# Optimization experiments

Measured on AMD Instinct MI355X. Metric: run time of the kernel, lower is better.

The kernel has to match this reference:

```python
import jax, jax.numpy as jnp
import numpy as np

B, N, OBS = 512, 64, 256
H1, H2 = 4, 4
D = 128            # embed/key dim (d_k_1 = d_k_2 = 128)
O1 = D // H1       # 32, per-head value dim stage 1
O2 = D // H2       # 32, per-head value dim stage 2
IN2 = O1 * H1      # 128, input dim to stage 2
FOUT = 16          # final_output_dim


def setup_inputs() -> dict:
    key = jax.random.key(0)
    ks = jax.random.split(key, 22)
    g = lambda k, shp: (jax.random.normal(k, shp, dtype=jnp.float32) * 0.05)
    inp = {
        "states": jax.random.normal(ks[0], (B, N, OBS), dtype=jnp.float32),
        # stage 1 per-head params, stacked over heads
        "E1_w": g(ks[1], (H1, D, OBS)), "E1_b": g(ks[2], (H1, D)),
        "K1_w": g(ks[3], (H1, D, D)),   "K1_b": g(ks[4], (H1, D)),
        "Q1_w": g(ks[5], (H1, D, D)),   "Q1_b": g(ks[6], (H1, D)),
        "V1_w": g(ks[7], (H1, O1, D)),  "V1_b": g(ks[8], (H1, O1)),
        # stage 2 per-head params
        "E2_w": g(ks[9], (H2, D, IN2)), "E2_b": g(ks[10], (H2, D)),
        "K2_w": g(ks[11], (H2, D, D)),  "K2_b": g(ks[12], (H2, D)),
        "Q2_w": g(ks[13], (H2, D, D)),  "Q2_b": g(ks[14], (H2, D)),
        "V2_w": g(ks[15], (H2, O2, D)), "V2_b": g(ks[16], (H2, O2)),
        # final MLP policy head
        "F1_w": g(ks[17], (64, O2 * H2)), "F1_b": g(ks[18], (64,)),
        "F2_w": g(ks[19], (FOUT, 64)),    "F2_b": g(ks[20], (FOUT,)),
    }
    return inp


def _attn_block(x, Ew, Eb, Kw, Kb, Qw, Qb, Vw, Vb, d_k):
    # x: [B,N,I]; all head loops batched via leading head axis h
    se = jax.nn.leaky_relu(jnp.einsum('bni,hdi->hbnd', x, Ew) + Eb[:, None, None, :])  # [h,B,N,D]
    k = jnp.einsum('hbnd,hed->hbne', se, Kw) + Kb[:, None, None, :]
    q = jnp.einsum('hbnd,hed->hbne', se, Qw) + Qb[:, None, None, :]
    w = jax.nn.softmax(jnp.einsum('hbne,hbme->hbnm', q, k) / jnp.sqrt(jnp.float32(d_k)), axis=-1)  # [h,B,N,N]
    v = jax.nn.leaky_relu(jnp.einsum('hbnd,hod->hbno', se, Vw) + Vb[:, None, None, :])  # [h,B,N,O]
    att = jnp.einsum('hbnm,hbmo->hbno', w, v)
    h, b, n, o = att.shape
    return jnp.transpose(att, (1, 2, 0, 3)).reshape(b, n, h * o), w


def reference(states, E1_w, E1_b, K1_w, K1_b, Q1_w, Q1_b, V1_w, V1_b,
              E2_w, E2_b, K2_w, K2_b, Q2_w, Q2_b, V2_w, V2_b,
              F1_w, F1_b, F2_w, F2_b):
    x1, w1 = _attn_block(states, E1_w, E1_b, K1_w, K1_b, Q1_w, Q1_b, V1_w, V1_b, D)
    x2, w2 = _attn_block(x1, E2_w, E2_b, K2_w, K2_b, Q2_w, Q2_b, V2_w, V2_b, D)
    h = jax.nn.leaky_relu(jnp.einsum('bnf,of->bno', x2, F1_w) + F1_b)
    policy = jax.nn.softmax(jnp.einsum('bno,po->bnp', h, F2_w) + F2_b, axis=-1)
    return policy, w1, w2
```

## Files before the change

kernel.cpp:

```cpp
#include <hip/hip_runtime.h>

typedef __attribute__((ext_vector_type(8))) short short8;
typedef __attribute__((ext_vector_type(4))) short short4v;
typedef __attribute__((ext_vector_type(4))) float f32x4;
typedef __attribute__((ext_vector_type(2))) unsigned uint2v;

#define MFMA(a, b, c) __builtin_amdgcn_mfma_f32_16x16x32_bf16((a), (b), (c), 0, 0, 0)

__device__ __forceinline__ short f2bf(float f) {
    union { float f; unsigned u; } v; v.f = f;
    unsigned r = v.u + 0x7fffu + ((v.u >> 16) & 1u);
    return (short)(r >> 16);
}
__device__ __forceinline__ float bf2f(short s) {
    union { unsigned u; float f; } v; v.u = ((unsigned)(unsigned short)s) << 16; return v.f;
}
__device__ __forceinline__ unsigned pkbf(float lo, float hi) {
    return (unsigned)(unsigned short)f2bf(lo) | ((unsigned)(unsigned short)f2bf(hi) << 16);
}
__device__ __forceinline__ float lrelu(float v) { return (v >= 0.f) ? v : 0.01f * v; }

struct ConvArgs { const float* src[6]; int end[6]; };

__global__ __launch_bounds__(256) void convert_weights_kernel(ConvArgs a, short* __restrict__ dstw) {
    int i4 = blockIdx.x * 256 + threadIdx.x;
    int seg = 0;
#pragma unroll
    for (int s = 0; s < 5; s++) seg += (i4 >= a.end[s]) ? 1 : 0;
    int base = (seg == 0) ? 0 : a.end[seg - 1];
    float4 v = ((const float4*)a.src[seg])[i4 - base];
    uint2v o = { pkbf(v.x, v.y), pkbf(v.z, v.w) };
    *(uint2v*)(dstw + (size_t)i4 * 4) = o;
}

__global__ __launch_bounds__(256) void precompute_gt_kernel(
    const float* __restrict__ Q1w, const float* __restrict__ K1w, const float* __restrict__ Q1b,
    const float* __restrict__ Q2w, const float* __restrict__ K2w, const float* __restrict__ Q2b,
    short* __restrict__ gt, float* __restrict__ wvec) {
    const int s  = blockIdx.x >> 5;
    const int h  = (blockIdx.x >> 3) & 3;
    const int fg = blockIdx.x & 7;
    const float* Qw = (s ? Q2w : Q1w) + (size_t)h * 16384;
    const float* Kw = (s ? K2w : K1w) + (size_t)h * 16384;
    const float* qb = (s ? Q2b : Q1b) + h * 128;
    const int f  = fg * 16 + (threadIdx.x >> 4);
    const int e0 = (threadIdx.x & 15) * 8;
    float acc[8] = {0.f, 0.f, 0.f, 0.f, 0.f, 0.f, 0.f, 0.f};
    float accw = 0.f;
#pragma unroll 4
    for (int c = 0; c < 128; c++) {
        float kv = Kw[c * 128 + f];
        accw = fmaf(qb[c], kv, accw);
        float4 a0 = *(const float4*)(Qw + c * 128 + e0);
        float4 a1 = *(const float4*)(Qw + c * 128 + e0 + 4);
        acc[0] = fmaf(kv, a0.x, acc[0]); acc[1] = fmaf(kv, a0.y, acc[1]);
        acc[2] = fmaf(kv, a0.z, acc[2]); acc[3] = fmaf(kv, a0.w, acc[3]);
        acc[4] = fmaf(kv, a1.x, acc[4]); acc[5] = fmaf(kv, a1.y, acc[5]);
        acc[6] = fmaf(kv, a1.z, acc[6]); acc[7] = fmaf(kv, a1.w, acc[7]);
    }
    const float scale = 0.08838834764831845f;
    short8 o = { f2bf(acc[0] * scale), f2bf(acc[1] * scale), f2bf(acc[2] * scale), f2bf(acc[3] * scale),
                 f2bf(acc[4] * scale), f2bf(acc[5] * scale), f2bf(acc[6] * scale), f2bf(acc[7] * scale) };
    *(short8*)(gt + ((size_t)((s * 4 + h) * 128 + f)) * 128 + e0) = o;
    if (e0 == 0) wvec[(s * 4 + h) * 128 + f] = accw * scale;
}

template<int IN, bool XF32>
__global__ __launch_bounds__(256, XF32 ? 3 : 4) void attn_stage_kernel(
    const void* __restrict__ xin,
    const short* __restrict__ Ew, const float* __restrict__ Eb,
    const short* __restrict__ Gt, const float* __restrict__ wvec,
    const short* __restrict__ Vw, const float* __restrict__ Vb,
    float* __restrict__ w_out,
    short* __restrict__ x_out)
{
    constexpr int XLD   = IN + 8;
    constexpr int OFF_X = 0;
    constexpr int OFF_T = 0;
    constexpr int OFF_VT = 8704;
    constexpr int OFF_CB = 11008;
    constexpr int OFF_W  = 0;
    constexpr int OFF_SE = (64 * XLD > 11136) ? 64 * XLD : 11136;
    __shared__ short sm[OFF_SE + 64 * 136];

    const int tid  = threadIdx.x;
    const int b    = blockIdx.x & 511;
    const int h    = blockIdx.x >> 9;
    const int wv   = tid >> 6;
    const int lane = tid & 63;
    const int quad = lane >> 4;
    const int l16  = lane & 15;
    constexpr int NK1 = IN / 32;

    if constexpr (XF32) {
        const float* xb = (const float*)xin + (size_t)b * 64 * IN;
#pragma unroll
        for (int r = 0; r < IN / 16; r++) {
            int f4 = tid + 256 * r;
            int row = f4 / (IN / 4), c4 = f4 % (IN / 4);
            float4 v = ((const float4*)xb)[f4];
            uint2v o = { pkbf(v.x, v.y), pkbf(v.z, v.w) };
            *(uint2v*)&sm[OFF_X + row * XLD + c4 * 4] = o;
        }
    } else {
        const short* xb = (const short*)xin + (size_t)b * 64 * IN;
#pragma unroll
        for (int r = 0; r < IN / 32; r++) {
            int f8 = tid + 256 * r;
            int row = f8 / (IN / 8), c8 = f8 % (IN / 8);
            short8 v = *(const short8*)(xb + (size_t)f8 * 8);
            *(short8*)&sm[OFF_X + row * XLD + c8 * 8] = v;
        }
    }

    short8 ebf[NK1 * 2];
    {
        const short* ewh = Ew + (size_t)h * 128 * IN;
#pragma unroll
        for (int k0i = 0; k0i < NK1; k0i++)
#pragma unroll
            for (int j = 0; j < 2; j++)
                ebf[k0i * 2 + j] = *(const short8*)(ewh + (size_t)(wv * 32 + j * 16 + l16) * IN + k0i * 32 + quad * 8);
    }
    __syncthreads();

    short8 gtf[8];

    {
        f32x4 acc[4][2];
#pragma unroll
        for (int j = 0; j < 2; j++) {
            f32x4 eb4 = *(const f32x4*)&Eb[h * 128 + wv * 32 + j * 16 + quad * 4];
#pragma unroll
            for (int i = 0; i < 4; i++) acc[i][j] = eb4;
        }
        __builtin_amdgcn_s_setprio(1);
#pragma unroll
        for (int k0i = 0; k0i < NK1; k0i++) {
            short8 x8[4];
#pragma unroll
            for (int i = 0; i < 4; i++)
                x8[i] = *(const short8*)&sm[OFF_X + (i * 16 + l16) * XLD + k0i * 32 + quad * 8];
#pragma unroll
            for (int i = 0; i < 4; i++)
#pragma unroll
                for (int j = 0; j < 2; j++)
                    acc[i][j] = MFMA(ebf[k0i * 2 + j], x8[i], acc[i][j]);
        }
        __builtin_amdgcn_s_setprio(0);
        {
            const short* gth = Gt + (size_t)h * 16384;
#pragma unroll
            for (int k0i = 0; k0i < 4; k0i++)
#pragma unroll
                for (int j = 0; j < 2; j++)
                    gtf[k0i * 2 + j] = *(const short8*)(gth + (size_t)(wv * 32 + j * 16 + l16) * 128 + k0i * 32 + quad * 8);
        }
#pragma unroll
        for (int i = 0; i < 4; i++)
#pragma unroll
            for (int j = 0; j < 2; j++) {
                uint2v o = { pkbf(lrelu(acc[i][j][0]), lrelu(acc[i][j][1])),
                             pkbf(lrelu(acc[i][j][2]), lrelu(acc[i][j][3])) };
                *(uint2v*)&sm[OFF_SE + (i * 16 + l16) * 136 + wv * 32 + j * 16 + quad * 4] = o;
            }
    }
    __syncthreads();

    {
        f32x4 tacc[4][2];
        f32x4 z = {0.f, 0.f, 0.f, 0.f};
#pragma unroll
        for (int i = 0; i < 4; i++)
#pragma unroll
            for (int j = 0; j < 2; j++) tacc[i][j] = z;
        __builtin_amdgcn_s_setprio(1);
#pragma unroll
        for (int k0i = 0; k0i < 4; k0i++) {
            short8 se8[4];
#pragma unroll
            for (int i = 0; i < 4; i++)
                se8[i] = *(const short8*)&sm[OFF_SE + (i * 16 + l16) * 136 + k0i * 32 + quad * 8];
#pragma unroll
            for (int i = 0; i < 4; i++)
#pragma unroll
                for (int j = 0; j < 2; j++)
                    tacc[i][j] = MFMA(gtf[k0i * 2 + j], se8[i], tacc[i][j]);
        }
#pragma unroll
        for (int i = 0; i < 4; i++)
#pragma unroll
            for (int j = 0; j < 2; j++) {
                uint2v o = { pkbf(tacc[i][j][0], tacc[i][j][1]),
                             pkbf(tacc[i][j][2], tacc[i][j][3]) };
                *(uint2v*)&sm[OFF_T + (i * 16 + l16) * 136 + wv * 32 + j * 16 + quad * 4] = o;
            }

        const short* vwh = Vw + (size_t)h * 32 * 128;
        const int n0v = (wv >> 1) * 16, mrow = (wv & 1) * 32;
        short8 vbf[4];
#pragma unroll
        for (int k0i = 0; k0i < 4; k0i++)
            vbf[k0i] = *(const short8*)(vwh + (size_t)(n0v + l16) * 128 + k0i * 32 + quad * 8);
        float vb = Vb[h * 32 + n0v + l16];
        f32x4 vacc[2];
        vacc[0] = (f32x4){vb, vb, vb, vb}; vacc[1] = vacc[0];
#pragma unroll
        for (int k0i = 0; k0i < 4; k0i++) {
            short8 a0 = *(const short8*)&sm[OFF_SE + (mrow + l16) * 136 + k0i * 32 + quad * 8];
            short8 a1 = *(const short8*)&sm[OFF_SE + (mrow + 16 + l16) * 136 + k0i * 32 + quad * 8];
            vacc[0] = MFMA(a0, vbf[k0i], vacc[0]);
            vacc[1] = MFMA(a1, vbf[k0i], vacc[1]);
        }
        __builtin_amdgcn_s_setprio(0);
#pragma unroll
        for (int i = 0; i < 2; i++) {
            uint2v o = { pkbf(lrelu(vacc[i][0]), lrelu(vacc[i][1])),
                         pkbf(lrelu(vacc[i][2]), lrelu(vacc[i][3])) };
            *(uint2v*)&sm[OFF_VT + (n0v + l16) * 72 + mrow + i * 16 + quad * 4] = o;
        }

        {
            const float* wvh = wvec + h * 128;
            const int row = wv * 16 + (lane >> 2);
            const int e0 = (lane & 3) * 32;
            float s = 0.f;
#pragma unroll
            for (int u = 0; u < 32; u += 8) {
                short8 sv = *(const short8*)&sm[OFF_SE + row * 136 + e0 + u];
                float4 w0 = *(const float4*)(wvh + e0 + u);
                float4 w1 = *(const float4*)(wvh + e0 + u + 4);
                s = fmaf(bf2f(sv[0]), w0.x, s); s = fmaf(bf2f(sv[1]), w0.y, s);
                s = fmaf(bf2f(sv[2]), w0.z, s); s = fmaf(bf2f(sv[3]), w0.w, s);
                s = fmaf(bf2f(sv[4]), w1.x, s); s = fmaf(bf2f(sv[5]), w1.y, s);
                s = fmaf(bf2f(sv[6]), w1.z, s); s = fmaf(bf2f(sv[7]), w1.w, s);
            }
            s += __shfl_xor(s, 1, 4);
            s += __shfl_xor(s, 2, 4);
            if ((lane & 3) == 0) ((float*)&sm[OFF_CB])[row] = s;
        }
    }
    __syncthreads();

    f32x4 lacc[4];
#pragma unroll
    for (int jj = 0; jj < 4; jj++) lacc[jj] = (f32x4){0.f, 0.f, 0.f, 0.f};
    __builtin_amdgcn_s_setprio(1);
#pragma unroll
    for (int k0 = 0; k0 < 128; k0 += 32) {
        short8 t8 = *(const short8*)&sm[OFF_T + (wv * 16 + l16) * 136 + k0 + quad * 8];
#pragma unroll
        for (int jj = 0; jj < 4; jj++) {
            short8 se8 = *(const short8*)&sm[OFF_SE + (jj * 16 + l16) * 136 + k0 + quad * 8];
            lacc[jj] = MFMA(se8, t8, lacc[jj]);
        }
    }
    __builtin_amdgcn_s_setprio(0);
    __syncthreads();

    {
        const float* cbf = (const float*)&sm[OFF_CB];
#pragma unroll
        for (int jj = 0; jj < 4; jj++) {
            f32x4 cb4 = *(const f32x4*)&cbf[jj * 16 + quad * 4];
            lacc[jj] += cb4;
        }
        float m01 = fmaxf(fmaxf(lacc[0][0], lacc[0][1]), fmaxf(lacc[0][2], lacc[0][3]));
        float m23 = fmaxf(fmaxf(lacc[1][0], lacc[1][1]), fmaxf(lacc[1][2], lacc[1][3]));
        float m45 = fmaxf(fmaxf(lacc[2][0], lacc[2][1]), fmaxf(lacc[2][2], lacc[2][3]));
        float m67 = fmaxf(fmaxf(lacc[3][0], lacc[3][1]), fmaxf(lacc[3][2], lacc[3][3]));
        float m = fmaxf(fmaxf(m01, m23), fmaxf(m45, m67));
        m = fmaxf(m, __shfl_xor(m, 16, 64));
        m = fmaxf(m, __shfl_xor(m, 32, 64));
        float sum = 0.f;
#pragma unroll
        for (int jj = 0; jj < 4; jj++)
#pragma unroll
            for (int r = 0; r < 4; r++) {
                float e = __expf(lacc[jj][r] - m);
                lacc[jj][r] = e; sum += e;
            }
        sum += __shfl_xor(sum, 16, 64);
        sum += __shfl_xor(sum, 32, 64);
        float inv = 1.0f / sum;
        float* wbase = w_out + ((size_t)(h * 512 + b)) * 4096 + (size_t)(wv * 16 + l16) * 64;
#pragma unroll
        for (int jj = 0; jj < 4; jj++) {
            f32x4 w4 = { lacc[jj][0] * inv, lacc[jj][1] * inv, lacc[jj][2] * inv, lacc[jj][3] * inv };
            uint2v o = { pkbf(w4[0], w4[1]), pkbf(w4[2], w4[3]) };
            *(uint2v*)&sm[OFF_W + (wv * 16 + l16) * 72 + jj * 16 + quad * 4] = o;
            __builtin_nontemporal_store(w4, (f32x4*)(wbase + jj * 16 + quad * 4));
        }
    }
    __syncthreads();

    {
        f32x4 aacc[2]; aacc[0] = (f32x4){0.f, 0.f, 0.f, 0.f}; aacc[1] = aacc[0];
#pragma unroll
        for (int k0 = 0; k0 < 64; k0 += 32) {
            short8 w8 = *(const short8*)&sm[OFF_W + (wv * 16 + l16) * 72 + k0 + quad * 8];
#pragma unroll
            for (int j = 0; j < 2; j++) {
                short8 v8 = *(const short8*)&sm[OFF_VT + (j * 16 + l16) * 72 + k0 + quad * 8];
                aacc[j] = MFMA(v8, w8, aacc[j]);
            }
        }
        short* xob = x_out + (size_t)b * 64 * 128 + (size_t)(wv * 16 + l16) * 128 + h * 32;
#pragma unroll
        for (int j = 0; j < 2; j++) {
            uint2v o = { pkbf(aacc[j][0], aacc[j][1]), pkbf(aacc[j][2], aacc[j][3]) };
            *(uint2v*)&xob[j * 16 + quad * 4] = o;
        }
    }
}

#define H_LD 72
__global__ __launch_bounds__(256)
void final_mlp_mfma_kernel(const short* __restrict__ x2,
                           const short* __restrict__ F1wb,
                           const float* __restrict__ F1b,
                           const short* __restrict__ F2wb,
                           const float* __restrict__ F2b,
                           float* __restrict__ policy)
{
    __shared__ short hsm[4][16 * H_LD];
    const int tid  = threadIdx.x;
    const int wv   = tid >> 6;
    const int lane = tid & 63;
    const int quad = lane >> 4;
    const int l16  = lane & 15;
    const int rowbase = blockIdx.x * 64 + wv * 16;

    short8 a[4];
    const short* xrow = x2 + (size_t)(rowbase + l16) * 128;
#pragma unroll
    for (int k = 0; k < 4; k++) a[k] = *(const short8*)(xrow + k * 32 + quad * 8);
    f32x4 acc[4];
#pragma unroll
    for (int j = 0; j < 4; j++) acc[j] = *(const f32x4*)&F1b[j * 16 + quad * 4];
#pragma unroll
    for (int k = 0; k < 4; k++)
#pragma unroll
        for (int j = 0; j < 4; j++) {
            short8 b8 = *(const short8*)(F1wb + (size_t)(j * 16 + l16) * 128 + k * 32 + quad * 8);
            acc[j] = MFMA(b8, a[k], acc[j]);
        }
    short* hh = &hsm[wv][0];
#pragma unroll
    for (int j = 0; j < 4; j++) {
        uint2v o = { pkbf(lrelu(acc[j][0]), lrelu(acc[j][1])),
                     pkbf(lrelu(acc[j][2]), lrelu(acc[j][3])) };
        *(uint2v*)&hh[l16 * H_LD + j * 16 + quad * 4] = o;
    }
    __syncthreads();

    f32x4 lg = *(const f32x4*)&F2b[quad * 4];
#pragma unroll
    for (int k = 0; k < 2; k++) {
        short8 a2 = *(const short8*)(hh + l16 * H_LD + k * 32 + quad * 8);
        short8 b2 = *(const short8*)(F2wb + (size_t)l16 * 64 + k * 32 + quad * 8);
        lg = MFMA(b2, a2, lg);
    }
    float m = fmaxf(fmaxf(lg[0], lg[1]), fmaxf(lg[2], lg[3]));
    m = fmaxf(m, __shfl_xor(m, 16, 64));
    m = fmaxf(m, __shfl_xor(m, 32, 64));
    f32x4 e;
    float s = 0.f;
#pragma unroll
    for (int r = 0; r < 4; r++) { e[r] = __expf(lg[r] - m); s += e[r]; }
    s += __shfl_xor(s, 16, 64);
    s += __shfl_xor(s, 32, 64);
    float inv = 1.0f / s;
    f32x4 p4 = { e[0] * inv, e[1] * inv, e[2] * inv, e[3] * inv };
    __builtin_nontemporal_store(p4, (f32x4*)&policy[(size_t)(rowbase + l16) * 16 + quad * 4]);
}

extern "C" void kernel_launch(void* const* d_in, const int* in_sizes, int n_in,
                              void* d_out, int out_size, void* d_ws, size_t ws_size,
                              hipStream_t stream) {
    const float* states = (const float*)d_in[0];
    const float* E1w = (const float*)d_in[1];  const float* E1b = (const float*)d_in[2];
    const float* K1w = (const float*)d_in[3];  const float* K1b = (const float*)d_in[4];
    const float* Q1w = (const float*)d_in[5];  const float* Q1b = (const float*)d_in[6];
    const float* V1w = (const float*)d_in[7];  const float* V1b = (const float*)d_in[8];
    const float* E2w = (const float*)d_in[9];  const float* E2b = (const float*)d_in[10];
    const float* K2w = (const float*)d_in[11]; const float* K2b = (const float*)d_in[12];
    const float* Q2w = (const float*)d_in[13]; const float* Q2b = (const float*)d_in[14];
    const float* V2w = (const float*)d_in[15]; const float* V2b = (const float*)d_in[16];
    const float* F1w = (const float*)d_in[17]; const float* F1b = (const float*)d_in[18];
    const float* F2w = (const float*)d_in[19]; const float* F2b = (const float*)d_in[20];
    (void)K1b; (void)K2b;

    float* out    = (float*)d_out;
    float* policy = out;
    float* w1     = out + 512 * 64 * 16;
    float* w2     = w1 + 4 * 512 * 64 * 64;

    short* wsb = (short*)d_ws;
    short* x1b = wsb;
    short* x2b = wsb + 4194304;
    short* wts = wsb + 8388608;
    short* wE1 = wts;
    short* wV1 = wts + 131072;
    short* wE2 = wts + 147456;
    short* wV2 = wts + 212992;
    short* wF1 = wts + 229376;
    short* wF2 = wts + 237568;
    short* gt  = wts + 238592;
    float* wvec = (float*)(wts + 238592 + 131072);

    ConvArgs ca;
    ca.src[0] = E1w; ca.src[1] = V1w; ca.src[2] = E2w; ca.src[3] = V2w;
    ca.src[4] = F1w; ca.src[5] = F2w;
    ca.end[0] = 32768;  ca.end[1] = 36864;  ca.end[2] = 53248;  ca.end[3] = 57344;
    ca.end[4] = 59392;  ca.end[5] = 59648;
    convert_weights_kernel<<<233, 256, 0, stream>>>(ca, wts);
    precompute_gt_kernel<<<64, 256, 0, stream>>>(Q1w, K1w, Q1b, Q2w, K2w, Q2b, gt, wvec);

    attn_stage_kernel<256, true><<<2048, 256, 0, stream>>>(
        (const void*)states, wE1, E1b, gt, wvec, wV1, V1b, w1, x1b);
    attn_stage_kernel<128, false><<<2048, 256, 0, stream>>>(
        (const void*)x1b, wE2, E2b, gt + 65536, wvec + 512, wV2, V2b, w2, x2b);
    final_mlp_mfma_kernel<<<512, 256, 0, stream>>>(x2b, wF1, F1b, wF2, F2b, policy);
}
```

Measured before the change: 233.1 us.

## Make each wave own 16 rows and stream x and weights from global

Each wave now computes all 128 embedding columns for its own 16 rows. The input rows are read straight from global memory into MFMA fragments instead of being staged in shared memory, and the E, G and V weight fragments are loaded per MFMA rather than held in registers. Removing the X staging buffer shrinks shared memory, which allows 4 blocks per CU for the fp32 stage as well, and because the T and W tiles are now row-local one barrier is dropped. The cost is more global and L2 traffic for weights, since each wave reloads the full weight matrices.

```diff
diff --git a/kernel.cpp b/kernel.cpp
--- a/kernel.cpp
+++ b/kernel.cpp
@@ -1,7 +1,6 @@
 #include <hip/hip_runtime.h>
 
 typedef __attribute__((ext_vector_type(8))) short short8;
-typedef __attribute__((ext_vector_type(4))) short short4v;
 typedef __attribute__((ext_vector_type(4))) float f32x4;
 typedef __attribute__((ext_vector_type(2))) unsigned uint2v;
 
@@ -66,7 +65,7 @@
 }
 
 template<int IN, bool XF32>
-__global__ __launch_bounds__(256, XF32 ? 3 : 4) void attn_stage_kernel(
+__global__ __launch_bounds__(256, 4) void attn_stage_kernel(
     const void* __restrict__ xin,
     const short* __restrict__ Ew, const float* __restrict__ Eb,
     const short* __restrict__ Gt, const float* __restrict__ wvec,
@@ -74,14 +73,11 @@
     float* __restrict__ w_out,
     short* __restrict__ x_out)
 {
-    constexpr int XLD   = IN + 8;
-    constexpr int OFF_X = 0;
-    constexpr int OFF_T = 0;
-    constexpr int OFF_VT = 8704;
-    constexpr int OFF_CB = 11008;
-    constexpr int OFF_W  = 0;
-    constexpr int OFF_SE = (64 * XLD > 11136) ? 64 * XLD : 11136;
-    __shared__ short sm[OFF_SE + 64 * 136];
+    constexpr int OFF_T  = 0;
+    constexpr int OFF_SE = 8704;
+    constexpr int OFF_VT = 17408;
+    constexpr int OFF_CB = 19712;
+    __shared__ short sm[19840];
 
     const int tid  = threadIdx.x;
     const int b    = blockIdx.x & 511;
@@ -90,134 +86,84 @@
     const int lane = tid & 63;
     const int quad = lane >> 4;
     const int l16  = lane & 15;
+    const int myrow = wv * 16 + l16;
     constexpr int NK1 = IN / 32;
 
-    if constexpr (XF32) {
-        const float* xb = (const float*)xin + (size_t)b * 64 * IN;
-#pragma unroll
-        for (int r = 0; r < IN / 16; r++) {
-            int f4 = tid + 256 * r;
-            int row = f4 / (IN / 4), c4 = f4 % (IN / 4);
-            float4 v = ((const float4*)xb)[f4];
-            uint2v o = { pkbf(v.x, v.y), pkbf(v.z, v.w) };
-            *(uint2v*)&sm[OFF_X + row * XLD + c4 * 4] = o;
-        }
-    } else {
-        const short* xb = (const short*)xin + (size_t)b * 64 * IN;
-#pragma unroll
-        for (int r = 0; r < IN / 32; r++) {
-            int f8 = tid + 256 * r;
-            int row = f8 / (IN / 8), c8 = f8 % (IN / 8);
-            short8 v = *(const short8*)(xb + (size_t)f8 * 8);
-            *(short8*)&sm[OFF_X + row * XLD + c8 * 8] = v;
-        }
-    }
-
-    short8 ebf[NK1 * 2];
     {
         const short* ewh = Ew + (size_t)h * 128 * IN;
-#pragma unroll
-        for (int k0i = 0; k0i < NK1; k0i++)
-#pragma unroll
-            for (int j = 0; j < 2; j++)
-                ebf[k0i * 2 + j] = *(const short8*)(ewh + (size_t)(wv * 32 + j * 16 + l16) * IN + k0i * 32 + quad * 8);
+        f32x4 acc[8];
+#pragma unroll
+        for (int e = 0; e < 8; e++) acc[e] = *(const f32x4*)&Eb[h * 128 + e * 16 + quad * 4];
+#pragma unroll
+        for (int k0i = 0; k0i < NK1; k0i++) {
+            short8 xf;
+            if constexpr (XF32) {
+                const float* xp = (const float*)xin + ((size_t)b * 64 + myrow) * IN + k0i * 32 + quad * 8;
+                float4 a0 = *(const float4*)xp;
+                float4 a1 = *(const float4*)(xp + 4);
+                union { unsigned u[4]; short8 s; } xu;
+                xu.u[0] = pkbf(a0.x, a0.y); xu.u[1] = pkbf(a0.z, a0.w);
+                xu.u[2] = pkbf(a1.x, a1.y); xu.u[3] = pkbf(a1.z, a1.w);
+                xf = xu.s;
+            } else {
+                xf = *(const short8*)((const short*)xin + ((size_t)b * 64 + myrow) * IN + k0i * 32 + quad * 8);
+            }
+#pragma unroll
+            for (int e = 0; e < 8; e++) {
+                short8 ef = *(const short8*)(ewh + (size_t)(e * 16 + l16) * IN + k0i * 32 + quad * 8);
+                acc[e] = MFMA(ef, xf, acc[e]);
+            }
+        }
+#pragma unroll
+        for (int e = 0; e < 8; e++) {
+            uint2v o = { pkbf(lrelu(acc[e][0]), lrelu(acc[e][1])),
+                         pkbf(lrelu(acc[e][2]), lrelu(acc[e][3])) };
+            *(uint2v*)&sm[OFF_SE + myrow * 136 + e * 16 + quad * 4] = o;
+        }
     }
     __syncthreads();
 
-    short8 gtf[8];
-
     {
-        f32x4 acc[4][2];
-#pragma unroll
-        for (int j = 0; j < 2; j++) {
-            f32x4 eb4 = *(const f32x4*)&Eb[h * 128 + wv * 32 + j * 16 + quad * 4];
-#pragma unroll
-            for (int i = 0; i < 4; i++) acc[i][j] = eb4;
-        }
+        short8 sf[4];
+#pragma unroll
+        for (int k0i = 0; k0i < 4; k0i++)
+            sf[k0i] = *(const short8*)&sm[OFF_SE + myrow * 136 + k0i * 32 + quad * 8];
+
+        const short* gth = Gt + (size_t)h * 16384;
+        f32x4 tacc[8];
+#pragma unroll
+        for (int f = 0; f < 8; f++) tacc[f] = (f32x4){0.f, 0.f, 0.f, 0.f};
         __builtin_amdgcn_s_setprio(1);
 #pragma unroll
-        for (int k0i = 0; k0i < NK1; k0i++) {
-            short8 x8[4];
-#pragma unroll
-            for (int i = 0; i < 4; i++)
-                x8[i] = *(const short8*)&sm[OFF_X + (i * 16 + l16) * XLD + k0i * 32 + quad * 8];
-#pragma unroll
-            for (int i = 0; i < 4; i++)
-#pragma unroll
-                for (int j = 0; j < 2; j++)
-                    acc[i][j] = MFMA(ebf[k0i * 2 + j], x8[i], acc[i][j]);
-        }
+        for (int k0i = 0; k0i < 4; k0i++)
+#pragma unroll
+            for (int f = 0; f < 8; f++) {
+                short8 gf = *(const short8*)(gth + (size_t)(f * 16 + l16) * 128 + k0i * 32 + quad * 8);
+                tacc[f] = MFMA(gf, sf[k0i], tacc[f]);
+            }
+#pragma unroll
+        for (int f = 0; f < 8; f++) {
+            uint2v ot = { pkbf(tacc[f][0], tacc[f][1]), pkbf(tacc[f][2], tacc[f][3]) };
+            *(uint2v*)&sm[OFF_T + myrow * 136 + f * 16 + quad * 4] = ot;
+        }
+
+        const short* vwh = Vw + (size_t)h * 32 * 128;
+        f32x4 vacc[2];
+#pragma unroll
+        for (int o = 0; o < 2; o++) { float bv = Vb[h * 32 + o * 16 + l16]; vacc[o] = (f32x4){bv, bv, bv, bv}; }
+#pragma unroll
+        for (int k0i = 0; k0i < 4; k0i++)
+#pragma unroll
+            for (int o = 0; o < 2; o++) {
+                short8 vb8 = *(const short8*)(vwh + (size_t)(o * 16 + l16) * 128 + k0i * 32 + quad * 8);
+                vacc[o] = MFMA(sf[k0i], vb8, vacc[o]);
+            }
         __builtin_amdgcn_s_setprio(0);
-        {
-            const short* gth = Gt + (size_t)h * 16384;
-#pragma unroll
-            for (int k0i = 0; k0i < 4; k0i++)
-#pragma unroll
-                for (int j = 0; j < 2; j++)
-                    gtf[k0i * 2 + j] = *(const short8*)(gth + (size_t)(wv * 32 + j * 16 + l16) * 128 + k0i * 32 + quad * 8);
-        }
-#pragma unroll
-        for (int i = 0; i < 4; i++)
-#pragma unroll
-            for (int j = 0; j < 2; j++) {
-                uint2v o = { pkbf(lrelu(acc[i][j][0]), lrelu(acc[i][j][1])),
-                             pkbf(lrelu(acc[i][j][2]), lrelu(acc[i][j][3])) };
-                *(uint2v*)&sm[OFF_SE + (i * 16 + l16) * 136 + wv * 32 + j * 16 + quad * 4] = o;
-            }
-    }
-    __syncthreads();
-
-    {
-        f32x4 tacc[4][2];
-        f32x4 z = {0.f, 0.f, 0.f, 0.f};
-#pragma unroll
-        for (int i = 0; i < 4; i++)
-#pragma unroll
-            for (int j = 0; j < 2; j++) tacc[i][j] = z;
-        __builtin_amdgcn_s_setprio(1);
-#pragma unroll
-        for (int k0i = 0; k0i < 4; k0i++) {
-            short8 se8[4];
-#pragma unroll
-            for (int i = 0; i < 4; i++)
-                se8[i] = *(const short8*)&sm[OFF_SE + (i * 16 + l16) * 136 + k0i * 32 + quad * 8];
-#pragma unroll
-            for (int i = 0; i < 4; i++)
-#pragma unroll
-                for (int j = 0; j < 2; j++)
-                    tacc[i][j] = MFMA(gtf[k0i * 2 + j], se8[i], tacc[i][j]);
-        }
-#pragma unroll
-        for (int i = 0; i < 4; i++)
-#pragma unroll
-            for (int j = 0; j < 2; j++) {
-                uint2v o = { pkbf(tacc[i][j][0], tacc[i][j][1]),
-                             pkbf(tacc[i][j][2], tacc[i][j][3]) };
-                *(uint2v*)&sm[OFF_T + (i * 16 + l16) * 136 + wv * 32 + j * 16 + quad * 4] = o;
-            }
-
-        const short* vwh = Vw + (size_t)h * 32 * 128;
-        const int n0v = (wv >> 1) * 16, mrow = (wv & 1) * 32;
-        short8 vbf[4];
-#pragma unroll
-        for (int k0i = 0; k0i < 4; k0i++)
-            vbf[k0i] = *(const short8*)(vwh + (size_t)(n0v + l16) * 128 + k0i * 32 + quad * 8);
-        float vb = Vb[h * 32 + n0v + l16];
-        f32x4 vacc[2];
-        vacc[0] = (f32x4){vb, vb, vb, vb}; vacc[1] = vacc[0];
-#pragma unroll
-        for (int k0i = 0; k0i < 4; k0i++) {
-            short8 a0 = *(const short8*)&sm[OFF_SE + (mrow + l16) * 136 + k0i * 32 + quad * 8];
-            short8 a1 = *(const short8*)&sm[OFF_SE + (mrow + 16 + l16) * 136 + k0i * 32 + quad * 8];
-            vacc[0] = MFMA(a0, vbf[k0i], vacc[0]);
-            vacc[1] = MFMA(a1, vbf[k0i], vacc[1]);
-        }
-        __builtin_amdgcn_s_setprio(0);
-#pragma unroll
-        for (int i = 0; i < 2; i++) {
-            uint2v o = { pkbf(lrelu(vacc[i][0]), lrelu(vacc[i][1])),
-                         pkbf(lrelu(vacc[i][2]), lrelu(vacc[i][3])) };
-            *(uint2v*)&sm[OFF_VT + (n0v + l16) * 72 + mrow + i * 16 + quad * 4] = o;
+#pragma unroll
+        for (int o = 0; o < 2; o++) {
+            uint2v ov = { pkbf(lrelu(vacc[o][0]), lrelu(vacc[o][1])),
+                          pkbf(lrelu(vacc[o][2]), lrelu(vacc[o][3])) };
+            *(uint2v*)&sm[OFF_VT + (o * 16 + l16) * 72 + wv * 16 + quad * 4] = ov;
         }
 
         {
@@ -248,15 +194,14 @@
     __builtin_amdgcn_s_setprio(1);
 #pragma unroll
     for (int k0 = 0; k0 < 128; k0 += 32) {
-        short8 t8 = *(const short8*)&sm[OFF_T + (wv * 16 + l16) * 136 + k0 + quad * 8];
+        short8 tf = *(const short8*)&sm[OFF_T + myrow * 136 + k0 + quad * 8];
 #pragma unroll
         for (int jj = 0; jj < 4; jj++) {
-            short8 se8 = *(const short8*)&sm[OFF_SE + (jj * 16 + l16) * 136 + k0 + quad * 8];
-            lacc[jj] = MFMA(se8, t8, lacc[jj]);
+            short8 af = *(const short8*)&sm[OFF_SE + (jj * 16 + l16) * 136 + k0 + quad * 8];
+            lacc[jj] = MFMA(af, tf, lacc[jj]);
         }
     }
     __builtin_amdgcn_s_setprio(0);
-    __syncthreads();
 
     {
         const float* cbf = (const float*)&sm[OFF_CB];
@@ -283,12 +228,12 @@
         sum += __shfl_xor(sum, 16, 64);
         sum += __shfl_xor(sum, 32, 64);
         float inv = 1.0f / sum;
-        float* wbase = w_out + ((size_t)(h * 512 + b)) * 4096 + (size_t)(wv * 16 + l16) * 64;
+        float* wbase = w_out + ((size_t)(h * 512 + b)) * 4096 + (size_t)myrow * 64;
 #pragma unroll
         for (int jj = 0; jj < 4; jj++) {
             f32x4 w4 = { lacc[jj][0] * inv, lacc[jj][1] * inv, lacc[jj][2] * inv, lacc[jj][3] * inv };
             uint2v o = { pkbf(w4[0], w4[1]), pkbf(w4[2], w4[3]) };
-            *(uint2v*)&sm[OFF_W + (wv * 16 + l16) * 72 + jj * 16 + quad * 4] = o;
+            *(uint2v*)&sm[OFF_T + myrow * 136 + jj * 16 + quad * 4] = o;
             __builtin_nontemporal_store(w4, (f32x4*)(wbase + jj * 16 + quad * 4));
         }
     }
@@ -298,18 +243,18 @@
         f32x4 aacc[2]; aacc[0] = (f32x4){0.f, 0.f, 0.f, 0.f}; aacc[1] = aacc[0];
 #pragma unroll
         for (int k0 = 0; k0 < 64; k0 += 32) {
-            short8 w8 = *(const short8*)&sm[OFF_W + (wv * 16 + l16) * 72 + k0 + quad * 8];
-#pragma unroll
-            for (int j = 0; j < 2; j++) {
-                short8 v8 = *(const short8*)&sm[OFF_VT + (j * 16 + l16) * 72 + k0 + quad * 8];
-                aacc[j] = MFMA(v8, w8, aacc[j]);
-            }
-        }
-        short* xob = x_out + (size_t)b * 64 * 128 + (size_t)(wv * 16 + l16) * 128 + h * 32;
-#pragma unroll
-        for (int j = 0; j < 2; j++) {
-            uint2v o = { pkbf(aacc[j][0], aacc[j][1]), pkbf(aacc[j][2], aacc[j][3]) };
-            *(uint2v*)&xob[j * 16 + quad * 4] = o;
+            short8 wf = *(const short8*)&sm[OFF_T + myrow * 136 + k0 + quad * 8];
+#pragma unroll
+            for (int o = 0; o < 2; o++) {
+                short8 vf = *(const short8*)&sm[OFF_VT + (o * 16 + l16) * 72 + k0 + quad * 8];
+                aacc[o] = MFMA(vf, wf, aacc[o]);
+            }
+        }
+        short* xob = x_out + (size_t)b * 8192 + (size_t)myrow * 128 + h * 32;
+#pragma unroll
+        for (int o = 0; o < 2; o++) {
+            uint2v o8 = { pkbf(aacc[o][0], aacc[o][1]), pkbf(aacc[o][2], aacc[o][3]) };
+            *(uint2v*)&xob[o * 16 + quad * 4] = o8;
         }
     }
 }
```

After: 351.6 us. +50.8%, slower.

## Pre-convert states to bf16 and stage inputs via direct global-to-LDS swizzled loads

Applied to the files above, without the earlier changes.

Moves the fp32-to-bf16 conversion of the states tensor into the weight-conversion kernel, writing a bf16 copy to workspace. Both attention stages can then load inputs with global_load_lds straight into an XOR-swizzled unpadded LDS layout. The LDS plan is reworked so buffers alias, the attention weights reuse the T buffer, and two __syncthreads are dropped. The precompute kernel is also re-parallelized over more blocks. The cost is an extra full pass over states (write bf16, read again) plus possible hazards from the removed barriers, since aliased buffers are written by other waves.

```diff
diff --git a/kernel.cpp b/kernel.cpp
--- a/kernel.cpp
+++ b/kernel.cpp
@@ -1,7 +1,6 @@
 #include <hip/hip_runtime.h>
 
 typedef __attribute__((ext_vector_type(8))) short short8;
-typedef __attribute__((ext_vector_type(4))) short short4v;
 typedef __attribute__((ext_vector_type(4))) float f32x4;
 typedef __attribute__((ext_vector_type(2))) unsigned uint2v;
 
@@ -20,68 +19,67 @@
 }
 __device__ __forceinline__ float lrelu(float v) { return (v >= 0.f) ? v : 0.01f * v; }
 
-struct ConvArgs { const float* src[6]; int end[6]; };
-
-__global__ __launch_bounds__(256) void convert_weights_kernel(ConvArgs a, short* __restrict__ dstw) {
+__device__ __forceinline__ void load_lds16(const void* g, void* l) {
+    __builtin_amdgcn_global_load_lds((const __attribute__((address_space(1))) void*)g,
+                                     (__attribute__((address_space(3))) void*)l, 16, 0, 0);
+}
+
+struct ConvArgs { const float* src[7]; int end[7]; };
+
+__global__ __launch_bounds__(256) void convert_weights_kernel(ConvArgs a,
+                                                              short* __restrict__ dstw,
+                                                              short* __restrict__ dstx) {
     int i4 = blockIdx.x * 256 + threadIdx.x;
     int seg = 0;
 #pragma unroll
-    for (int s = 0; s < 5; s++) seg += (i4 >= a.end[s]) ? 1 : 0;
+    for (int s = 0; s < 6; s++) seg += (i4 >= a.end[s]) ? 1 : 0;
     int base = (seg == 0) ? 0 : a.end[seg - 1];
     float4 v = ((const float4*)a.src[seg])[i4 - base];
     uint2v o = { pkbf(v.x, v.y), pkbf(v.z, v.w) };
-    *(uint2v*)(dstw + (size_t)i4 * 4) = o;
+    short* dst = (seg == 6) ? (dstx + (size_t)(i4 - a.end[5]) * 4)
+                            : (dstw + (size_t)i4 * 4);
+    *(uint2v*)dst = o;
 }
 
 __global__ __launch_bounds__(256) void precompute_gt_kernel(
     const float* __restrict__ Q1w, const float* __restrict__ K1w, const float* __restrict__ Q1b,
     const float* __restrict__ Q2w, const float* __restrict__ K2w, const float* __restrict__ Q2b,
     short* __restrict__ gt, float* __restrict__ wvec) {
-    const int s  = blockIdx.x >> 5;
-    const int h  = (blockIdx.x >> 3) & 3;
-    const int fg = blockIdx.x & 7;
+    const int s  = blockIdx.x >> 8;
+    const int h  = (blockIdx.x >> 6) & 3;
+    const int fg = blockIdx.x & 63;
     const float* Qw = (s ? Q2w : Q1w) + (size_t)h * 16384;
     const float* Kw = (s ? K2w : K1w) + (size_t)h * 16384;
     const float* qb = (s ? Q2b : Q1b) + h * 128;
-    const int f  = fg * 16 + (threadIdx.x >> 4);
-    const int e0 = (threadIdx.x & 15) * 8;
-    float acc[8] = {0.f, 0.f, 0.f, 0.f, 0.f, 0.f, 0.f, 0.f};
-    float accw = 0.f;
-#pragma unroll 4
+    const int f = fg * 2 + (threadIdx.x >> 7);
+    const int e = threadIdx.x & 127;
+    float acc = 0.f, accw = 0.f;
+#pragma unroll 8
     for (int c = 0; c < 128; c++) {
         float kv = Kw[c * 128 + f];
+        acc  = fmaf(Qw[c * 128 + e], kv, acc);
         accw = fmaf(qb[c], kv, accw);
-        float4 a0 = *(const float4*)(Qw + c * 128 + e0);
-        float4 a1 = *(const float4*)(Qw + c * 128 + e0 + 4);
-        acc[0] = fmaf(kv, a0.x, acc[0]); acc[1] = fmaf(kv, a0.y, acc[1]);
-        acc[2] = fmaf(kv, a0.z, acc[2]); acc[3] = fmaf(kv, a0.w, acc[3]);
-        acc[4] = fmaf(kv, a1.x, acc[4]); acc[5] = fmaf(kv, a1.y, acc[5]);
-        acc[6] = fmaf(kv, a1.z, acc[6]); acc[7] = fmaf(kv, a1.w, acc[7]);
     }
     const float scale = 0.08838834764831845f;
-    short8 o = { f2bf(acc[0] * scale), f2bf(acc[1] * scale), f2bf(acc[2] * scale), f2bf(acc[3] * scale),
-                 f2bf(acc[4] * scale), f2bf(acc[5] * scale), f2bf(acc[6] * scale), f2bf(acc[7] * scale) };
-    *(short8*)(gt + ((size_t)((s * 4 + h) * 128 + f)) * 128 + e0) = o;
-    if (e0 == 0) wvec[(s * 4 + h) * 128 + f] = accw * scale;
-}
-
-template<int IN, bool XF32>
-__global__ __launch_bounds__(256, XF32 ? 3 : 4) void attn_stage_kernel(
-    const void* __restrict__ xin,
+    gt[((size_t)((s * 4 + h) * 128 + f)) * 128 + e] = f2bf(acc * scale);
+    if (e == 0) wvec[(s * 4 + h) * 128 + f] = accw * scale;
+}
+
+template<int IN>
+__global__ __launch_bounds__(256, (IN == 256) ? 3 : 4) void attn_stage_kernel(
+    const short* __restrict__ xin,
     const short* __restrict__ Ew, const float* __restrict__ Eb,
     const short* __restrict__ Gt, const float* __restrict__ wvec,
     const short* __restrict__ Vw, const float* __restrict__ Vb,
     float* __restrict__ w_out,
     short* __restrict__ x_out)
 {
-    constexpr int XLD   = IN + 8;
-    constexpr int OFF_X = 0;
-    constexpr int OFF_T = 0;
-    constexpr int OFF_VT = 8704;
-    constexpr int OFF_CB = 11008;
-    constexpr int OFF_W  = 0;
-    constexpr int OFF_SE = (64 * XLD > 11136) ? 64 * XLD : 11136;
-    __shared__ short sm[OFF_SE + 64 * 136];
+    constexpr int OFF_T  = 0;
+    constexpr int OFF_SE = 64 * IN;
+    constexpr int OFF_VT = (IN == 256) ? 8192 : (64 * IN + 8704);
+    constexpr int OFF_CB = OFF_VT + 2304;
+    constexpr int SMEM   = (IN == 256) ? 25088 : 19328;
+    __shared__ short sm[SMEM];
 
     const int tid  = threadIdx.x;
     const int b    = blockIdx.x & 511;
@@ -90,26 +88,18 @@
     const int lane = tid & 63;
     const int quad = lane >> 4;
     const int l16  = lane & 15;
+    const int myrow = wv * 16 + l16;
     constexpr int NK1 = IN / 32;
 
-    if constexpr (XF32) {
-        const float* xb = (const float*)xin + (size_t)b * 64 * IN;
-#pragma unroll
-        for (int r = 0; r < IN / 16; r++) {
-            int f4 = tid + 256 * r;
-            int row = f4 / (IN / 4), c4 = f4 % (IN / 4);
-            float4 v = ((const float4*)xb)[f4];
-            uint2v o = { pkbf(v.x, v.y), pkbf(v.z, v.w) };
-            *(uint2v*)&sm[OFF_X + row * XLD + c4 * 4] = o;
-        }
-    } else {
-        const short* xb = (const short*)xin + (size_t)b * 64 * IN;
-#pragma unroll
-        for (int r = 0; r < IN / 32; r++) {
-            int f8 = tid + 256 * r;
-            int row = f8 / (IN / 8), c8 = f8 % (IN / 8);
-            short8 v = *(const short8*)(xb + (size_t)f8 * 8);
-            *(short8*)&sm[OFF_X + row * XLD + c8 * 8] = v;
+    {
+        const short* xg = xin + (size_t)b * 64 * IN;
+#pragma unroll
+        for (int t = 0; t < IN / 32; t++) {
+            int off   = wv * 16 * IN + t * 512 + lane * 8;
+            int row   = off / IN;
+            int chunk = (off % IN) >> 3;
+            int src   = row * IN + ((chunk ^ (row & 7)) << 3);
+            load_lds16(xg + src, &sm[wv * 16 * IN + t * 512]);
         }
     }
 
@@ -139,8 +129,11 @@
         for (int k0i = 0; k0i < NK1; k0i++) {
             short8 x8[4];
 #pragma unroll
-            for (int i = 0; i < 4; i++)
-                x8[i] = *(const short8*)&sm[OFF_X + (i * 16 + l16) * XLD + k0i * 32 + quad * 8];
+            for (int i = 0; i < 4; i++) {
+                int xrow = i * 16 + l16;
+                int kc = k0i * 4 + quad;
+                x8[i] = *(const short8*)&sm[xrow * IN + ((kc ^ (xrow & 7)) << 3)];
+            }
 #pragma unroll
             for (int i = 0; i < 4; i++)
 #pragma unroll
@@ -191,9 +184,11 @@
         for (int i = 0; i < 4; i++)
 #pragma unroll
             for (int j = 0; j < 2; j++) {
-                uint2v o = { pkbf(tacc[i][j][0], tacc[i][j][1]),
-                             pkbf(tacc[i][j][2], tacc[i][j][3]) };
-                *(uint2v*)&sm[OFF_T + (i * 16 + l16) * 136 + wv * 32 + j * 16 + quad * 4] = o;
+                uint2v ot = { pkbf(tacc[i][j][0], tacc[i][j][1]),
+                              pkbf(tacc[i][j][2], tacc[i][j][3]) };
+                int trow = i * 16 + l16;
+                int c = wv * 4 + j * 2 + (quad >> 1);
+                *(uint2v*)&sm[OFF_T + trow * 128 + ((c ^ (trow & 7)) << 3) + (quad & 1) * 4] = ot;
             }
 
         const short* vwh = Vw + (size_t)h * 32 * 128;
@@ -215,9 +210,9 @@
         __builtin_amdgcn_s_setprio(0);
 #pragma unroll
         for (int i = 0; i < 2; i++) {
-            uint2v o = { pkbf(lrelu(vacc[i][0]), lrelu(vacc[i][1])),
-                         pkbf(lrelu(vacc[i][2]), lrelu(vacc[i][3])) };
-            *(uint2v*)&sm[OFF_VT + (n0v + l16) * 72 + mrow + i * 16 + quad * 4] = o;
+            uint2v ov = { pkbf(lrelu(vacc[i][0]), lrelu(vacc[i][1])),
+                          pkbf(lrelu(vacc[i][2]), lrelu(vacc[i][3])) };
+            *(uint2v*)&sm[OFF_VT + (n0v + l16) * 72 + mrow + i * 16 + quad * 4] = ov;
         }
 
         {
@@ -248,15 +243,15 @@
     __builtin_amdgcn_s_setprio(1);
 #pragma unroll
     for (int k0 = 0; k0 < 128; k0 += 32) {
-        short8 t8 = *(const short8*)&sm[OFF_T + (wv * 16 + l16) * 136 + k0 + quad * 8];
+        int kc = (k0 >> 3) + quad;
+        short8 tf = *(const short8*)&sm[OFF_T + myrow * 128 + ((kc ^ (myrow & 7)) << 3)];
 #pragma unroll
         for (int jj = 0; jj < 4; jj++) {
-            short8 se8 = *(const short8*)&sm[OFF_SE + (jj * 16 + l16) * 136 + k0 + quad * 8];
-            lacc[jj] = MFMA(se8, t8, lacc[jj]);
+            short8 af = *(const short8*)&sm[OFF_SE + (jj * 16 + l16) * 136 + k0 + quad * 8];
+            lacc[jj] = MFMA(af, tf, lacc[jj]);
         }
     }
     __builtin_amdgcn_s_setprio(0);
-    __syncthreads();
 
     {
         const float* cbf = (const float*)&sm[OFF_CB];
@@ -283,33 +278,34 @@
         sum += __shfl_xor(sum, 16, 64);
         sum += __shfl_xor(sum, 32, 64);
         float inv = 1.0f / sum;
-        float* wbase = w_out + ((size_t)(h * 512 + b)) * 4096 + (size_t)(wv * 16 + l16) * 64;
+        float* wbase = w_out + ((size_t)(h * 512 + b)) * 4096 + (size_t)myrow * 64;
 #pragma unroll
         for (int jj = 0; jj < 4; jj++) {
             f32x4 w4 = { lacc[jj][0] * inv, lacc[jj][1] * inv, lacc[jj][2] * inv, lacc[jj][3] * inv };
             uint2v o = { pkbf(w4[0], w4[1]), pkbf(w4[2], w4[3]) };
-            *(uint2v*)&sm[OFF_W + (wv * 16 + l16) * 72 + jj * 16 + quad * 4] = o;
+            int c = jj * 2 + (quad >> 1);
+            *(uint2v*)&sm[OFF_T + myrow * 128 + ((c ^ (myrow & 7)) << 3) + (quad & 1) * 4] = o;
             __builtin_nontemporal_store(w4, (f32x4*)(wbase + jj * 16 + quad * 4));
         }
     }
-    __syncthreads();
 
     {
         f32x4 aacc[2]; aacc[0] = (f32x4){0.f, 0.f, 0.f, 0.f}; aacc[1] = aacc[0];
 #pragma unroll
         for (int k0 = 0; k0 < 64; k0 += 32) {
-            short8 w8 = *(const short8*)&sm[OFF_W + (wv * 16 + l16) * 72 + k0 + quad * 8];
-#pragma unroll
-            for (int j = 0; j < 2; j++) {
-                short8 v8 = *(const short8*)&sm[OFF_VT + (j * 16 + l16) * 72 + k0 + quad * 8];
-                aacc[j] = MFMA(v8, w8, aacc[j]);
-            }
-        }
-        short* xob = x_out + (size_t)b * 64 * 128 + (size_t)(wv * 16 + l16) * 128 + h * 32;
-#pragma unroll
-        for (int j = 0; j < 2; j++) {
-            uint2v o = { pkbf(aacc[j][0], aacc[j][1]), pkbf(aacc[j][2], aacc[j][3]) };
-            *(uint2v*)&xob[j * 16 + quad * 4] = o;
+            int kc = (k0 >> 3) + quad;
+            short8 wf = *(const short8*)&sm[OFF_T + myrow * 128 + ((kc ^ (myrow & 7)) << 3)];
+#pragma unroll
+            for (int o = 0; o < 2; o++) {
+                short8 vf = *(const short8*)&sm[OFF_VT + (o * 16 + l16) * 72 + k0 + quad * 8];
+                aacc[o] = MFMA(vf, wf, aacc[o]);
+            }
+        }
+        short* xob = x_out + (size_t)b * 8192 + (size_t)myrow * 128 + h * 32;
+#pragma unroll
+        for (int o = 0; o < 2; o++) {
+            uint2v o8 = { pkbf(aacc[o][0], aacc[o][1]), pkbf(aacc[o][2], aacc[o][3]) };
+            *(uint2v*)&xob[o * 16 + quad * 4] = o8;
         }
     }
 }
@@ -398,8 +394,9 @@
 
     short* wsb = (short*)d_ws;
     short* x1b = wsb;
-    short* x2b = wsb + 4194304;
-    short* wts = wsb + 8388608;
+    short* xsb = wsb + 4194304;
+    short* x2b = xsb;
+    short* wts = wsb + 12582912;
     short* wE1 = wts;
     short* wV1 = wts + 131072;
     short* wE2 = wts + 147456;
@@ -411,15 +408,15 @@
 
     ConvArgs ca;
     ca.src[0] = E1w; ca.src[1] = V1w; ca.src[2] = E2w; ca.src[3] = V2w;
-    ca.src[4] = F1w; ca.src[5] = F2w;
+    ca.src[4] = F1w; ca.src[5] = F2w; ca.src[6] = states;
     ca.end[0] = 32768;  ca.end[1] = 36864;  ca.end[2] = 53248;  ca.end[3] = 57344;
-    ca.end[4] = 59392;  ca.end[5] = 59648;
-    convert_weights_kernel<<<233, 256, 0, stream>>>(ca, wts);
-    precompute_gt_kernel<<<64, 256, 0, stream>>>(Q1w, K1w, Q1b, Q2w, K2w, Q2b, gt, wvec);
-
-    attn_stage_kernel<256, true><<<2048, 256, 0, stream>>>(
-        (const void*)states, wE1, E1b, gt, wvec, wV1, V1b, w1, x1b);
-    attn_stage_kernel<128, false><<<2048, 256, 0, stream>>>(
-        (const void*)x1b, wE2, E2b, gt + 65536, wvec + 512, wV2, V2b, w2, x2b);
+    ca.end[4] = 59392;  ca.end[5] = 59648;  ca.end[6] = 2156800;
+    convert_weights_kernel<<<8425, 256, 0, stream>>>(ca, wts, xsb);
+    precompute_gt_kernel<<<512, 256, 0, stream>>>(Q1w, K1w, Q1b, Q2w, K2w, Q2b, gt, wvec);
+
+    attn_stage_kernel<256><<<2048, 256, 0, stream>>>(
+        xsb, wE1, E1b, gt, wvec, wV1, V1b, w1, x1b);
+    attn_stage_kernel<128><<<2048, 256, 0, stream>>>(
+        x1b, wE2, E2b, gt + 65536, wvec + 512, wV2, V2b, w2, x2b);
     final_mlp_mfma_kernel<<<512, 256, 0, stream>>>(x2b, wF1, F1b, wF2, F2b, policy);
 }
```

Result: faster. 226.4 us (-2.9%).
